# Kernel optimization log

Hardware: AMD Instinct MI355X
Metric: run time of the kernel (lower is better)

## Reference

```python
import jax, jax.numpy as jnp
import numpy as np

D, H, W_IMG = 3, 128, 128
ZDIM, HDIM = 64, 512
KSEG, B = 8, 256
DIN = D * H * W_IMG


def setup_inputs() -> dict:
    key = jax.random.key(0)
    ks = jax.random.split(key, 18)
    s = 0.02
    inp = {
        "x": jax.random.normal(ks[0], (B, D, H, W_IMG), jnp.float32),
        "K": KSEG,
        "eps0": jax.random.normal(ks[1], (B, ZDIM), jnp.float32),
        "eps_q": jax.random.normal(ks[2], (KSEG - 1, B, ZDIM), jnp.float32),
        "eps_p": jax.random.normal(ks[3], (KSEG - 1, B, ZDIM), jnp.float32),
        # encoder stem (flattened image -> hdim) and gaussian head (hdim -> 2*zdim)
        "W_stem": jax.random.normal(ks[4], (DIN, HDIM), jnp.float32) * s,
        "b_stem": jnp.zeros((HDIM,), jnp.float32),
        "W_g": jax.random.normal(ks[5], (HDIM, 2 * ZDIM), jnp.float32) * s,
        "b_g": jnp.zeros((2 * ZDIM,), jnp.float32),
        # posterior LSTM (input zdim+hdim, hidden 2*zdim); initial state is always
        # zero in the original code (state is never fed back), so W_hh drops out.
        "Wih_q": jax.random.normal(ks[6], (ZDIM + HDIM, 8 * ZDIM), jnp.float32) * s,
        "b_q": jnp.zeros((8 * ZDIM,), jnp.float32),
        "Wlin_q": jax.random.normal(ks[7], (2 * ZDIM, 2 * ZDIM), jnp.float32) * s,
        "blin_q": jnp.zeros((2 * ZDIM,), jnp.float32),
        # prior LSTM (input zdim, hidden 2*zdim)
        "Wih_p": jax.random.normal(ks[8], (ZDIM, 8 * ZDIM), jnp.float32) * s,
        "b_p": jnp.zeros((8 * ZDIM,), jnp.float32),
        "Wlin_p": jax.random.normal(ks[9], (2 * ZDIM, 2 * ZDIM), jnp.float32) * s,
        "blin_p": jnp.zeros((2 * ZDIM,), jnp.float32),
        # decoder: zdim -> 1*h*w
        "W_dec": jax.random.normal(ks[10], (ZDIM, H * W_IMG), jnp.float32) * s,
        "b_dec": jnp.zeros((H * W_IMG,), jnp.float32),
    }
    return inp


def _std(logvar):
    return jax.nn.softplus(logvar + 0.5) + 1e-8


def _lstm_step_zero_state(xin, Wih, b):
    # single LSTM step with zero initial (h, c); W_hh contribution vanishes.
    g = xin @ Wih + b
    i, f, gg, o = jnp.split(g, 4, axis=-1)  # torch gate order i,f,g,o
    c = jax.nn.sigmoid(i) * jnp.tanh(gg)
    return jax.nn.sigmoid(o) * jnp.tanh(c)


def _kl_normal(mq, sq, mp, sp):
    return jnp.log(sp / sq) + (sq * sq + (mq - mp) ** 2) / (2.0 * sp * sp) - 0.5


def reference(x, K, eps0, eps_q, eps_p, W_stem, b_stem, W_g, b_g,
              Wih_q, b_q, Wlin_q, blin_q, Wih_p, b_p, Wlin_p, blin_p,
              W_dec, b_dec):
    batch = x.shape[0]
    xf = x.reshape(batch, -1)
    hf = jax.nn.relu(xf @ W_stem + b_stem)              # [B, hdim]
    enc = hf @ W_g + b_g
    mu, logvar = jnp.split(enc, 2, axis=1)
    s0 = _std(logvar)
    z0 = mu + s0 * eps0
    kl0 = -jnp.log(s0) + (s0 * s0 + mu * mu) / 2.0 - 0.5  # KL(q || N(0,1))

    def step(z_prev, eps_pair):
        eq, ep = eps_pair
        hq = _lstm_step_zero_state(jnp.concatenate([hf, z_prev], axis=1), Wih_q, b_q)
        enc_q = hq @ Wlin_q + blin_q
        mq, lq = jnp.split(enc_q, 2, axis=1)
        sq = _std(lq)
        zq = mq + sq * eq
        hp = _lstm_step_zero_state(z_prev, Wih_p, b_p)
        enc_p = hp @ Wlin_p + blin_p
        mp, lp = jnp.split(enc_p, 2, axis=1)
        sp = _std(lp)
        kl = _kl_normal(mq, sq, mp, sp)
        return zq, (zq, kl)

    _, (zq_s, kl_s) = jax.lax.scan(step, z0, (eps_q, eps_p))
    zs = jnp.concatenate([z0[None], zq_s], axis=0)       # [K, B, zdim]

    dec = (zs.reshape(K * batch, ZDIM) @ W_dec + b_dec)
    dec = dec.reshape(K, batch, 1, H, W_IMG)
    ls = jax.nn.log_sigmoid(dec)
    lns = jax.nn.log_sigmoid(-dec)
    log_ss_excl = jnp.cumsum(lns, axis=0) - lns          # exclusive prefix sum
    log_ms = log_ss_excl + ls                            # [K, B, 1, H, W]

    kl_all = jnp.concatenate([kl0[..., None], jnp.moveaxis(kl_s, 0, -1)], axis=-1)
    return log_ms, kl_all
```

## Files before the change

kernel.cpp:

```cpp
#include <hip/hip_runtime.h>
#include <hip/hip_bf16.h>

#define ZD 64
#define HD 512
#define NB 256
#define KS 8
#define DIN 49152
#define DN 16384

typedef __attribute__((ext_vector_type(8))) short bf16x8;
typedef __attribute__((ext_vector_type(4))) float f32x4;

__device__ __forceinline__ ushort bfc(float x) {
  uint u = __float_as_uint(x);
  uint r = (u + 0x7FFFu + ((u >> 16) & 1u)) >> 16;
  return (ushort)r;
}
__device__ __forceinline__ uint pk2(float a, float b) {
  return (uint)bfc(a) | ((uint)bfc(b) << 16);
}
__device__ __forceinline__ uint cvtpk(float lo, float hi) {
  uint r;
  asm("v_cvt_pk_bf16_f32 %0, %1, %2" : "=v"(r) : "v"(lo), "v"(hi));
  return r;
}
__device__ __forceinline__ float lof(uint u) { return __uint_as_float(u << 16); }
__device__ __forceinline__ float hif(uint u) { return __uint_as_float(u & 0xFFFF0000u); }
__device__ __forceinline__ float softplusf_(float x) {
  return fmaxf(x, 0.f) + log1pf(expf(-fabsf(x)));
}
__device__ __forceinline__ float softplus_fast(float x) {
  float e = __expf(-fabsf(x));
  return fmaxf(x, 0.f) + __logf(1.f + e);
}
__device__ __forceinline__ float sigmoidf_(float x) {
  return 1.f / (1.f + expf(-x));
}

#define SPLITS 128
#define KCH (DIN / SPLITS)
#define BKK 32

__global__ __launch_bounds__(256, 2)
void stem_kernel(const float* __restrict__ x, const float* __restrict__ W,
                 float* __restrict__ part) {
  __shared__ float Af[256 * 32];
  __shared__ uint Bt[128 * 20];
  const int id = blockIdx.x;
  const int nt = (id >> 3) & 3;
  const int sp = (id >> 5) * 8 + (id & 7);
  const int n0 = nt * 128;
  const int tid = threadIdx.x;
  const int lane = tid & 63;
  const int wave = tid >> 6;
  const int wm = wave >> 1, wn = wave & 1;
  const int rr = lane & 15, gq = lane >> 4;

  f32x4 accr[8][4];
#pragma unroll
  for (int i = 0; i < 8; ++i)
#pragma unroll
    for (int j = 0; j < 4; ++j) accr[i][j] = (f32x4){0.f, 0.f, 0.f, 0.f};

  const int arow_b = tid >> 3;
  const int asub = tid & 7;
  const int bkq = tid >> 5, bn4 = tid & 31;
  auto* ldsA = (__attribute__((address_space(3))) uint*)Af;

#pragma unroll 1
  for (int it = 0; it < KCH / BKK; ++it) {
    const int k0 = sp * KCH + it * BKK;
    __syncthreads();
#pragma unroll
    for (int i = 0; i < 8; ++i) {
      const int row = i * 32 + arow_b;
      const int slot = asub ^ (row & 7);
      const float* g = x + (size_t)row * DIN + k0 + slot * 4;
      __builtin_amdgcn_global_load_lds(
          (const __attribute__((address_space(1))) uint*)g,
          ldsA + i * 1024 + wave * 256, 16, 0, 0);
    }
    {
      float4 vb[4];
#pragma unroll
      for (int j = 0; j < 4; ++j)
        vb[j] = *(const float4*)(W + (size_t)(k0 + bkq * 4 + j) * HD + n0 + bn4 * 4);
      const int gg = bkq >> 1, sb = bkq & 1;
#pragma unroll
      for (int c = 0; c < 4; ++c) {
        const int n = bn4 * 4 + c;
        const float* q0 = (const float*)&vb[0];
        const float* q1 = (const float*)&vb[1];
        const float* q2 = (const float*)&vb[2];
        const float* q3 = (const float*)&vb[3];
        uint lo = cvtpk(q0[c], q1[c]);
        uint hi = cvtpk(q2[c], q3[c]);
        const int rot = (gg + (n >> 2) + n) & 3;
        *(uint2*)&Bt[n * 20 + rot * 4 + sb * 2] = make_uint2(lo, hi);
      }
    }
    asm volatile("s_waitcnt vmcnt(0)" ::: "memory");
    __syncthreads();
    bf16x8 af[8], bfr[4];
#pragma unroll
    for (int mf = 0; mf < 8; ++mf) {
      const int r = wm * 128 + mf * 16 + rr;
      const int s = r & 7;
      float4 a0 = *(const float4*)&Af[r * 32 + ((gq * 2) ^ s) * 4];
      float4 a1 = *(const float4*)&Af[r * 32 + ((gq * 2 + 1) ^ s) * 4];
      uint4 au = make_uint4(cvtpk(a0.x, a0.y), cvtpk(a0.z, a0.w),
                            cvtpk(a1.x, a1.y), cvtpk(a1.z, a1.w));
      af[mf] = *(bf16x8*)&au;
    }
#pragma unroll
    for (int nf = 0; nf < 4; ++nf) {
      const int n = wn * 64 + nf * 16 + rr;
      const int rot = (gq + (n >> 2) + n) & 3;
      uint4 bu = *(const uint4*)&Bt[n * 20 + rot * 4];
      bfr[nf] = *(bf16x8*)&bu;
    }
#pragma unroll
    for (int mf = 0; mf < 8; ++mf)
#pragma unroll
      for (int nf = 0; nf < 4; ++nf)
        accr[mf][nf] = __builtin_amdgcn_mfma_f32_16x16x32_bf16(
            af[mf], bfr[nf], accr[mf][nf], 0, 0, 0);
  }

  const int ccol = lane & 15, crow = (lane >> 4) * 4;
  float* base = part + (size_t)sp * (NB * HD);
#pragma unroll
  for (int mf = 0; mf < 8; ++mf) {
#pragma unroll
    for (int nf = 0; nf < 4; ++nf) {
      const int col = n0 + wn * 64 + nf * 16 + ccol;
      const int row = wm * 128 + mf * 16 + crow;
#pragma unroll
      for (int i = 0; i < 4; ++i)
        base[(size_t)(row + i) * HD + col] = accr[mf][nf][i];
    }
  }
}

__global__ __launch_bounds__(256)
void reduce_kernel(const float* __restrict__ part, float* __restrict__ acc) {
  const int idx = blockIdx.x * 256 + threadIdx.x;
  const float4* p = (const float4*)part;
  float4 s = p[idx];
#pragma unroll 8
  for (int sp = 1; sp < SPLITS; ++sp) {
    float4 v = p[(size_t)sp * (NB * HD / 4) + idx];
    s.x += v.x; s.y += v.y; s.z += v.z; s.w += v.w;
  }
  ((float4*)acc)[idx] = s;
}

__global__ __launch_bounds__(256)
void wcombT_kernel(const float* __restrict__ Wihq, const float* __restrict__ Wg,
                   ushort* __restrict__ WcT) {
  __shared__ float T[64][68];
  const int bx = blockIdx.x;
  const int by = blockIdx.y;
  const int t = threadIdx.x;
  const int ct = bx * 64, kt = by * 64;
  {
    const int rl = t >> 2, cq = (t & 3) * 16;
    const float* src = (bx < 8) ? &Wihq[(size_t)(kt + rl) * 512 + ct + cq]
                                : &Wg[(size_t)(kt + rl) * 128 + (ct - 512) + cq];
#pragma unroll
    for (int i = 0; i < 4; ++i) {
      float4 v = *(const float4*)(src + 4 * i);
      T[rl][cq + 4 * i + 0] = v.x;
      T[rl][cq + 4 * i + 1] = v.y;
      T[rl][cq + 4 * i + 2] = v.z;
      T[rl][cq + 4 * i + 3] = v.w;
    }
  }
  __syncthreads();
  {
    const int cl = t >> 2, kq = (t & 3) * 16;
    uint* dst = (uint*)WcT;
#pragma unroll
    for (int i = 0; i < 8; ++i) {
      uint u = pk2(T[kq + 2 * i][cl], T[kq + 2 * i + 1][cl]);
      dst[(((size_t)(ct + cl)) * 512 + kt + kq + 2 * i) >> 1] = u;
    }
  }
}

__global__ __launch_bounds__(256)
void gemmA_kernel(const float* __restrict__ acc, const float* __restrict__ bstem,
                  const ushort* __restrict__ WcT, const float* __restrict__ bq,
                  const float* __restrict__ bg, float* __restrict__ hfqg,
                  float* __restrict__ enc0g) {
  const int tid = threadIdx.x;
  const int lane = tid & 63;
  const int wave = tid >> 6;
  const int rr = lane & 15, gq = lane >> 4;
  const int mtile = blockIdx.y * 16;
  const int ncol = blockIdx.x * 64 + wave * 16;
  const int row = mtile + rr;

  f32x4 a4 = (f32x4){0.f, 0.f, 0.f, 0.f};
#pragma unroll
  for (int ks2 = 0; ks2 < 16; ++ks2) {
    const int k0 = ks2 * 32 + gq * 8;
    float4 x0 = *(const float4*)&acc[(size_t)row * HD + k0];
    float4 x1 = *(const float4*)&acc[(size_t)row * HD + k0 + 4];
    float4 b0 = *(const float4*)&bstem[k0];
    float4 b1 = *(const float4*)&bstem[k0 + 4];
    bf16x8 af;
    af[0] = (short)bfc(fmaxf(x0.x + b0.x, 0.f));
    af[1] = (short)bfc(fmaxf(x0.y + b0.y, 0.f));
    af[2] = (short)bfc(fmaxf(x0.z + b0.z, 0.f));
    af[3] = (short)bfc(fmaxf(x0.w + b0.w, 0.f));
    af[4] = (short)bfc(fmaxf(x1.x + b1.x, 0.f));
    af[5] = (short)bfc(fmaxf(x1.y + b1.y, 0.f));
    af[6] = (short)bfc(fmaxf(x1.z + b1.z, 0.f));
    af[7] = (short)bfc(fmaxf(x1.w + b1.w, 0.f));
    bf16x8 bf = *(const bf16x8*)&WcT[(size_t)(ncol + rr) * 512 + k0];
    a4 = __builtin_amdgcn_mfma_f32_16x16x32_bf16(af, bf, a4, 0, 0, 0);
  }
  const int col = ncol + rr;
  if (col < 512) {
    const float bb = bq[col];
#pragma unroll
    for (int i = 0; i < 4; ++i)
      hfqg[(size_t)(mtile + 4 * gq + i) * HD + col] = a4[i] + bb;
  } else {
    const float bb = bg[col - 512];
#pragma unroll
    for (int i = 0; i < 4; ++i)
      enc0g[(size_t)(mtile + 4 * gq + i) * 128 + (col - 512)] = a4[i] + bb;
  }
}

__global__ __launch_bounds__(512, 2)
void scan_kernel(const float* __restrict__ hfqg, const float* __restrict__ enc0g,
                 const float* __restrict__ Wihq, const float* __restrict__ Wihp,
                 const float* __restrict__ Wlinq, const float* __restrict__ blinq,
                 const float* __restrict__ Wlinp, const float* __restrict__ blinp,
                 const float* __restrict__ bp,
                 const float* __restrict__ eps0, const float* __restrict__ epsq,
                 ushort* __restrict__ zsb, float* __restrict__ out_kl) {
  const int b = blockIdx.x, tid = threadIdx.x;
  __shared__ uint WlL[2][64 * 128];
  __shared__ float g[512], gp[512];
  __shared__ float hq[128], hp[128];
  __shared__ float psum[512];
  __shared__ float zsh[64];
  __shared__ float epsL[448];

  uint wq[32], wp[32];
#pragma unroll
  for (int zp = 0; zp < 32; ++zp) {
    wq[zp] = pk2(Wihq[(size_t)(HD + 2 * zp) * HD + tid],
                 Wihq[(size_t)(HD + 2 * zp + 1) * HD + tid]);
    wp[zp] = pk2(Wihp[(size_t)(2 * zp) * HD + tid],
                 Wihp[(size_t)(2 * zp + 1) * HD + tid]);
  }
#pragma unroll
  for (int i = 0; i < 16; ++i) {
    int idx = i * 512 + tid;
    int kp2 = idx >> 7, jj = idx & 127;
    WlL[0][idx] = pk2(Wlinq[(2 * kp2) * 128 + jj], Wlinq[(2 * kp2 + 1) * 128 + jj]);
    WlL[1][idx] = pk2(Wlinp[(2 * kp2) * 128 + jj], Wlinp[(2 * kp2 + 1) * 128 + jj]);
  }
  if (tid < 448) epsL[tid] = epsq[(size_t)((tid >> 6) * NB + b) * ZD + (tid & 63)];
  const float hfq_reg = hfqg[(size_t)b * HD + tid];
  const float bp_reg = bp[tid];
  if (tid < 64) {
    float mu = enc0g[b * 128 + tid], lv = enc0g[b * 128 + 64 + tid];
    float s0 = softplusf_(lv + 0.5f) + 1e-8f;
    float z0 = mu + s0 * eps0[b * ZD + tid];
    zsh[tid] = z0;
    zsb[(b * KS) * ZD + tid] = bfc(z0);
    out_kl[(b * ZD + tid) * KS] = -logf(s0) + (s0 * s0 + mu * mu) * 0.5f - 0.5f;
  }
  __syncthreads();

  for (int t = 0; t < KS - 1; ++t) {
    float aq = hfq_reg, ap = bp_reg;
#pragma unroll
    for (int zp = 0; zp < 32; ++zp) {
      float z0v = zsh[2 * zp], z1v = zsh[2 * zp + 1];
      uint uq = wq[zp], up = wp[zp];
      aq += z0v * lof(uq) + z1v * hif(uq);
      ap += z0v * lof(up) + z1v * hif(up);
    }
    g[tid] = aq;
    gp[tid] = ap;
    __syncthreads();
    if (tid < 128) {
      float cs = sigmoidf_(g[tid]) * tanhf(g[256 + tid]);
      hq[tid] = sigmoidf_(g[384 + tid]) * tanhf(cs);
    } else if (tid < 256) {
      int j = tid & 127;
      float cs = sigmoidf_(gp[j]) * tanhf(gp[256 + j]);
      hp[j] = sigmoidf_(gp[384 + j]) * tanhf(cs);
    }
    __syncthreads();
    {
      int s = tid & 255, jj = s & 127, kc = s >> 7;
      int mq_ = tid >> 8;
      const float* h = mq_ ? hp : hq;
      const uint* W = WlL[mq_];
      float a = 0.f;
#pragma unroll
      for (int kp = 0; kp < 32; ++kp) {
        uint u = W[(kc * 32 + kp) * 128 + jj];
        a += h[kc * 64 + 2 * kp] * lof(u) + h[kc * 64 + 2 * kp + 1] * hif(u);
      }
      psum[tid] = a;
    }
    __syncthreads();
    if (tid < 64) {
      float mq = psum[tid] + psum[128 + tid] + blinq[tid];
      float lq = psum[64 + tid] + psum[192 + tid] + blinq[64 + tid];
      float sq = softplusf_(lq + 0.5f) + 1e-8f;
      float zq = mq + sq * epsL[t * 64 + tid];
      float mp2 = psum[256 + tid] + psum[384 + tid] + blinp[tid];
      float lp = psum[320 + tid] + psum[448 + tid] + blinp[64 + tid];
      float sp_ = softplusf_(lp + 0.5f) + 1e-8f;
      float d = mq - mp2;
      out_kl[(b * ZD + tid) * KS + t + 1] =
          logf(sp_ / sq) + (sq * sq + d * d) / (2.f * sp_ * sp_) - 0.5f;
      zsb[(b * KS + t + 1) * ZD + tid] = bfc(zq);
      zsh[tid] = zq;
    }
    __syncthreads();
  }
}

__global__ __launch_bounds__(256)
void wdt_kernel(const float* __restrict__ Wd, ushort* __restrict__ WdT) {
  const int c = blockIdx.x * 256 + threadIdx.x;
  uint packed[32];
#pragma unroll
  for (int k = 0; k < 32; ++k) {
    float a = Wd[(size_t)(2 * k) * DN + c];
    float b = Wd[(size_t)(2 * k + 1) * DN + c];
    packed[k] = pk2(a, b);
  }
  uint4* dst = (uint4*)&WdT[(size_t)c * 64];
#pragma unroll
  for (int i = 0; i < 8; ++i)
    dst[i] = make_uint4(packed[4 * i], packed[4 * i + 1], packed[4 * i + 2],
                        packed[4 * i + 3]);
}

__global__ __launch_bounds__(256)
void dec_kernel(const ushort* __restrict__ zsb, const ushort* __restrict__ WdT,
                const float* __restrict__ bd, float* __restrict__ out) {
  const int tid = threadIdx.x;
  const int lane = tid & 63;
  const int wave = tid >> 6;
  const int rr = lane & 15, gq = lane >> 4;
  const int mtile0 = blockIdx.y * 32;
  const int ncol0 = blockIdx.x * 256 + wave * 64;

  bf16x8 bfr[2][4];
#pragma unroll
  for (int ks2 = 0; ks2 < 2; ++ks2)
#pragma unroll
    for (int nf = 0; nf < 4; ++nf)
      bfr[ks2][nf] = *(const bf16x8*)&WdT[(size_t)(ncol0 + nf * 16 + rr) * 64 +
                                          ks2 * 32 + gq * 8];
  bf16x8 af[2][2];
#pragma unroll
  for (int mi = 0; mi < 2; ++mi)
#pragma unroll
    for (int ks2 = 0; ks2 < 2; ++ks2)
      af[mi][ks2] = *(const bf16x8*)&zsb[(size_t)(mtile0 + mi * 16 + rr) * 64 +
                                         ks2 * 32 + gq * 8];
  float bde[4];
#pragma unroll
  for (int nf = 0; nf < 4; ++nf) bde[nf] = bd[ncol0 + nf * 16 + rr];

  f32x4 acc[2][4];
#pragma unroll
  for (int mi = 0; mi < 2; ++mi)
#pragma unroll
    for (int nf = 0; nf < 4; ++nf) acc[mi][nf] = (f32x4){0.f, 0.f, 0.f, 0.f};

#pragma unroll
  for (int mi = 0; mi < 2; ++mi)
#pragma unroll
    for (int ks2 = 0; ks2 < 2; ++ks2)
#pragma unroll
      for (int nf = 0; nf < 4; ++nf)
        acc[mi][nf] = __builtin_amdgcn_mfma_f32_16x16x32_bf16(
            af[mi][ks2], bfr[ks2][nf], acc[mi][nf], 0, 0, 0);

  const int khi = (gq & 1) * 4;
#pragma unroll
  for (int mi = 0; mi < 2; ++mi) {
    const int bb = ((mtile0 + mi * 16) >> 3) + (gq >> 1);
#pragma unroll
    for (int nf = 0; nf < 4; ++nf) {
      const int col = ncol0 + nf * 16 + rr;
      float run = 0.f;
      float ov[4];
#pragma unroll
      for (int i = 0; i < 4; ++i) {
        float dec = acc[mi][nf][i] + bde[nf];
        float spd = softplus_fast(dec);
        ov[i] = run + (dec - spd);
        run -= spd;
      }
      float prev = __shfl_xor(run, 16, 64);
      float base = (gq & 1) ? prev : 0.f;
#pragma unroll
      for (int i = 0; i < 4; ++i)
        out[((size_t)(khi + i) * NB + bb) * DN + col] = ov[i] + base;
    }
  }
}

extern "C" void kernel_launch(void* const* d_in, const int* in_sizes, int n_in,
                              void* d_out, int out_size, void* d_ws, size_t ws_size,
                              hipStream_t stream) {
  (void)in_sizes; (void)n_in; (void)out_size; (void)ws_size;
  const float* x     = (const float*)d_in[0];
  const float* eps0  = (const float*)d_in[2];
  const float* epsq  = (const float*)d_in[3];
  const float* Wstem = (const float*)d_in[5];
  const float* bstem = (const float*)d_in[6];
  const float* Wg    = (const float*)d_in[7];
  const float* bgp   = (const float*)d_in[8];
  const float* Wihq  = (const float*)d_in[9];
  const float* bq    = (const float*)d_in[10];
  const float* Wlinq = (const float*)d_in[11];
  const float* blinq = (const float*)d_in[12];
  const float* Wihp  = (const float*)d_in[13];
  const float* bp    = (const float*)d_in[14];
  const float* Wlinp = (const float*)d_in[15];
  const float* blinp = (const float*)d_in[16];
  const float* Wd    = (const float*)d_in[17];
  const float* bd    = (const float*)d_in[18];

  float* out    = (float*)d_out;
  float* outkl  = out + (size_t)KS * NB * DN;
  float* accbuf = (float*)d_ws;
  ushort* zsb   = (ushort*)(accbuf + NB * HD);
  ushort* wdt   = zsb + (size_t)KS * NB * ZD;
  ushort* wcombT = wdt + (size_t)DN * ZD;
  float* hfqg   = (float*)(wcombT + 640 * 512);
  float* enc0g  = hfqg + NB * HD;
  float* part   = out;

  wdt_kernel<<<DN / 256, 256, 0, stream>>>(Wd, wdt);
  wcombT_kernel<<<dim3(10, 8), 256, 0, stream>>>(Wihq, Wg, wcombT);
  stem_kernel<<<4 * SPLITS, 256, 0, stream>>>(x, Wstem, part);
  reduce_kernel<<<NB * HD / 4 / 256, 256, 0, stream>>>(part, accbuf);
  gemmA_kernel<<<dim3(10, 16), 256, 0, stream>>>(accbuf, bstem, wcombT, bq, bgp,
                                                 hfqg, enc0g);
  scan_kernel<<<NB, 512, 0, stream>>>(hfqg, enc0g, Wihq, Wihp, Wlinq, blinq,
                                      Wlinp, blinp, bp, eps0, epsq, zsb, outkl);
  dec_kernel<<<dim3(64, 64), 256, 0, stream>>>(zsb, wdt, bd, out);
}
```

Before: 144.5 us.

## Halve stem split-K, merge weight prep kernels, pre-pack scan weights once

Cuts the stem split-K count from 128 to 64, so fewer partial buffers are written and reduced, and rewrites the reduce kernel so two half-blocks each sum 32 splits and combine through shared memory. Merges the decoder-weight transpose and the combined-weight transpose into a single prep kernel that also pre-packs the scan's LSTM and linear weights into bf16 once. Previously each of the 256 scan blocks converted these weights itself. This removes a launch and redundant conversion work, but each stem block now does a longer K loop and the grid has fewer blocks.

```diff
diff --git a/kernel.cpp b/kernel.cpp
--- a/kernel.cpp
+++ b/kernel.cpp
@@ -37,7 +37,7 @@
   return 1.f / (1.f + expf(-x));
 }
 
-#define SPLITS 128
+#define SPLITS 64
 #define KCH (DIN / SPLITS)
 #define BKK 32
 
@@ -144,46 +144,92 @@
 
 __global__ __launch_bounds__(256)
 void reduce_kernel(const float* __restrict__ part, float* __restrict__ acc) {
-  const int idx = blockIdx.x * 256 + threadIdx.x;
+  __shared__ float4 sh[128];
+  const int f4 = blockIdx.x * 128 + (threadIdx.x & 127);
+  const int half = threadIdx.x >> 7;
   const float4* p = (const float4*)part;
-  float4 s = p[idx];
+  float4 s = {0.f, 0.f, 0.f, 0.f};
 #pragma unroll 8
-  for (int sp = 1; sp < SPLITS; ++sp) {
-    float4 v = p[(size_t)sp * (NB * HD / 4) + idx];
+  for (int sp = half * 32; sp < half * 32 + 32; ++sp) {
+    float4 v = p[(size_t)sp * (NB * HD / 4) + f4];
     s.x += v.x; s.y += v.y; s.z += v.z; s.w += v.w;
   }
-  ((float4*)acc)[idx] = s;
+  if (half) sh[threadIdx.x - 128] = s;
+  __syncthreads();
+  if (!half) {
+    float4 o = sh[threadIdx.x];
+    o.x += s.x; o.y += s.y; o.z += s.z; o.w += s.w;
+    ((float4*)acc)[f4] = o;
+  }
 }
 
 __global__ __launch_bounds__(256)
-void wcombT_kernel(const float* __restrict__ Wihq, const float* __restrict__ Wg,
-                   ushort* __restrict__ WcT) {
+void prep_kernel(const float* __restrict__ Wd, ushort* __restrict__ WdT,
+                 const float* __restrict__ Wihq, const float* __restrict__ Wg,
+                 ushort* __restrict__ WcT,
+                 const float* __restrict__ Wihp,
+                 const float* __restrict__ Wlinq, const float* __restrict__ Wlinp,
+                 uint* __restrict__ wzq, uint* __restrict__ wzp,
+                 uint* __restrict__ wlq, uint* __restrict__ wlp) {
   __shared__ float T[64][68];
   const int bx = blockIdx.x;
-  const int by = blockIdx.y;
   const int t = threadIdx.x;
-  const int ct = bx * 64, kt = by * 64;
-  {
-    const int rl = t >> 2, cq = (t & 3) * 16;
-    const float* src = (bx < 8) ? &Wihq[(size_t)(kt + rl) * 512 + ct + cq]
-                                : &Wg[(size_t)(kt + rl) * 128 + (ct - 512) + cq];
-#pragma unroll
-    for (int i = 0; i < 4; ++i) {
-      float4 v = *(const float4*)(src + 4 * i);
-      T[rl][cq + 4 * i + 0] = v.x;
-      T[rl][cq + 4 * i + 1] = v.y;
-      T[rl][cq + 4 * i + 2] = v.z;
-      T[rl][cq + 4 * i + 3] = v.w;
-    }
-  }
-  __syncthreads();
-  {
-    const int cl = t >> 2, kq = (t & 3) * 16;
-    uint* dst = (uint*)WcT;
-#pragma unroll
-    for (int i = 0; i < 8; ++i) {
-      uint u = pk2(T[kq + 2 * i][cl], T[kq + 2 * i + 1][cl]);
-      dst[(((size_t)(ct + cl)) * 512 + kt + kq + 2 * i) >> 1] = u;
+  if (bx < 64) {
+    const int c = bx * 256 + t;
+    uint packed[32];
+#pragma unroll
+    for (int k = 0; k < 32; ++k) {
+      float a = Wd[(size_t)(2 * k) * DN + c];
+      float b = Wd[(size_t)(2 * k + 1) * DN + c];
+      packed[k] = pk2(a, b);
+    }
+    uint4* dst = (uint4*)&WdT[(size_t)c * 64];
+#pragma unroll
+    for (int i = 0; i < 8; ++i)
+      dst[i] = make_uint4(packed[4 * i], packed[4 * i + 1], packed[4 * i + 2],
+                          packed[4 * i + 3]);
+  } else if (bx < 144) {
+    const int bx2 = bx - 64;
+    const int cx = bx2 % 10, ky = bx2 / 10;
+    const int ct = cx * 64, kt = ky * 64;
+    {
+      const int rl = t >> 2, cq = (t & 3) * 16;
+      const float* src = (cx < 8) ? &Wihq[(size_t)(kt + rl) * 512 + ct + cq]
+                                  : &Wg[(size_t)(kt + rl) * 128 + (ct - 512) + cq];
+#pragma unroll
+      for (int i = 0; i < 4; ++i) {
+        float4 v = *(const float4*)(src + 4 * i);
+        T[rl][cq + 4 * i + 0] = v.x;
+        T[rl][cq + 4 * i + 1] = v.y;
+        T[rl][cq + 4 * i + 2] = v.z;
+        T[rl][cq + 4 * i + 3] = v.w;
+      }
+    }
+    __syncthreads();
+    {
+      const int cl = t >> 2, kq = (t & 3) * 16;
+      uint* dst = (uint*)WcT;
+#pragma unroll
+      for (int i = 0; i < 8; ++i) {
+        uint u = pk2(T[kq + 2 * i][cl], T[kq + 2 * i + 1][cl]);
+        dst[(((size_t)(ct + cl)) * 512 + kt + kq + 2 * i) >> 1] = u;
+      }
+    }
+  } else {
+    const int tp = (bx - 144) * 256 + t;
+#pragma unroll
+    for (int r2 = 0; r2 < 4; ++r2) {
+      const int i = tp * 4 + r2;
+      const int zp = i >> 9, col = i & 511;
+      wzq[i] = pk2(Wihq[(size_t)(HD + 2 * zp) * HD + col],
+                   Wihq[(size_t)(HD + 2 * zp + 1) * HD + col]);
+      wzp[i] = pk2(Wihp[(size_t)(2 * zp) * HD + col],
+                   Wihp[(size_t)(2 * zp + 1) * HD + col]);
+      if (i < 8192) {
+        const int kp2 = i >> 7, jj = i & 127;
+        wlq[i] = pk2(Wlinq[(2 * kp2) * 128 + jj], Wlinq[(2 * kp2 + 1) * 128 + jj]);
+        wlp[i] = pk2(Wlinp[(2 * kp2) * 128 + jj], Wlinp[(2 * kp2 + 1) * 128 + jj]);
+      }
     }
   }
 }
@@ -237,9 +283,9 @@
 
 __global__ __launch_bounds__(512, 2)
 void scan_kernel(const float* __restrict__ hfqg, const float* __restrict__ enc0g,
-                 const float* __restrict__ Wihq, const float* __restrict__ Wihp,
-                 const float* __restrict__ Wlinq, const float* __restrict__ blinq,
-                 const float* __restrict__ Wlinp, const float* __restrict__ blinp,
+                 const uint* __restrict__ wzqg, const uint* __restrict__ wzpg,
+                 const uint* __restrict__ wlqg, const uint* __restrict__ wlpg,
+                 const float* __restrict__ blinq, const float* __restrict__ blinp,
                  const float* __restrict__ bp,
                  const float* __restrict__ eps0, const float* __restrict__ epsq,
                  ushort* __restrict__ zsb, float* __restrict__ out_kl) {
@@ -254,17 +300,14 @@
   uint wq[32], wp[32];
 #pragma unroll
   for (int zp = 0; zp < 32; ++zp) {
-    wq[zp] = pk2(Wihq[(size_t)(HD + 2 * zp) * HD + tid],
-                 Wihq[(size_t)(HD + 2 * zp + 1) * HD + tid]);
-    wp[zp] = pk2(Wihp[(size_t)(2 * zp) * HD + tid],
-                 Wihp[(size_t)(2 * zp + 1) * HD + tid]);
+    wq[zp] = wzqg[zp * 512 + tid];
+    wp[zp] = wzpg[zp * 512 + tid];
   }
 #pragma unroll
   for (int i = 0; i < 16; ++i) {
-    int idx = i * 512 + tid;
-    int kp2 = idx >> 7, jj = idx & 127;
-    WlL[0][idx] = pk2(Wlinq[(2 * kp2) * 128 + jj], Wlinq[(2 * kp2 + 1) * 128 + jj]);
-    WlL[1][idx] = pk2(Wlinp[(2 * kp2) * 128 + jj], Wlinp[(2 * kp2 + 1) * 128 + jj]);
+    const int idx = i * 512 + tid;
+    WlL[0][idx] = wlqg[idx];
+    WlL[1][idx] = wlpg[idx];
   }
   if (tid < 448) epsL[tid] = epsq[(size_t)((tid >> 6) * NB + b) * ZD + (tid & 63)];
   const float hfq_reg = hfqg[(size_t)b * HD + tid];
@@ -330,23 +373,6 @@
     }
     __syncthreads();
   }
-}
-
-__global__ __launch_bounds__(256)
-void wdt_kernel(const float* __restrict__ Wd, ushort* __restrict__ WdT) {
-  const int c = blockIdx.x * 256 + threadIdx.x;
-  uint packed[32];
-#pragma unroll
-  for (int k = 0; k < 32; ++k) {
-    float a = Wd[(size_t)(2 * k) * DN + c];
-    float b = Wd[(size_t)(2 * k + 1) * DN + c];
-    packed[k] = pk2(a, b);
-  }
-  uint4* dst = (uint4*)&WdT[(size_t)c * 64];
-#pragma unroll
-  for (int i = 0; i < 8; ++i)
-    dst[i] = make_uint4(packed[4 * i], packed[4 * i + 1], packed[4 * i + 2],
-                        packed[4 * i + 3]);
 }
 
 __global__ __launch_bounds__(256)
@@ -447,15 +473,19 @@
   ushort* wcombT = wdt + (size_t)DN * ZD;
   float* hfqg   = (float*)(wcombT + 640 * 512);
   float* enc0g  = hfqg + NB * HD;
+  uint* wzq     = (uint*)(enc0g + NB * 128);
+  uint* wzp     = wzq + 32 * 512;
+  uint* wlq     = wzp + 32 * 512;
+  uint* wlp     = wlq + 64 * 128;
   float* part   = out;
 
-  wdt_kernel<<<DN / 256, 256, 0, stream>>>(Wd, wdt);
-  wcombT_kernel<<<dim3(10, 8), 256, 0, stream>>>(Wihq, Wg, wcombT);
+  prep_kernel<<<160, 256, 0, stream>>>(Wd, wdt, Wihq, Wg, wcombT, Wihp,
+                                       Wlinq, Wlinp, wzq, wzp, wlq, wlp);
   stem_kernel<<<4 * SPLITS, 256, 0, stream>>>(x, Wstem, part);
-  reduce_kernel<<<NB * HD / 4 / 256, 256, 0, stream>>>(part, accbuf);
+  reduce_kernel<<<NB * HD / 4 / 128, 256, 0, stream>>>(part, accbuf);
   gemmA_kernel<<<dim3(10, 16), 256, 0, stream>>>(accbuf, bstem, wcombT, bq, bgp,
                                                  hfqg, enc0g);
-  scan_kernel<<<NB, 512, 0, stream>>>(hfqg, enc0g, Wihq, Wihp, Wlinq, blinq,
-                                      Wlinp, blinp, bp, eps0, epsq, zsb, outkl);
+  scan_kernel<<<NB, 512, 0, stream>>>(hfqg, enc0g, wzq, wzp, wlq, wlp,
+                                      blinq, blinp, bp, eps0, epsq, zsb, outkl);
   dec_kernel<<<dim3(64, 64), 256, 0, stream>>>(zsb, wdt, bd, out);
 }
```

After: 144.6 us. About the same (+0.0%).
